# Optimization experiments

Hardware: AMD Instinct MI355X
Metric: run time of the kernel (lower is better)

The kernel has to match this reference:

```python
import jax, jax.numpy as jnp
import numpy as np

N, C, W = 64, 64, 4096
F, WW = 64, 9

def next_power2(n):
    return int(2 ** np.ceil(np.log2(n)))

def setup_inputs() -> dict:
    key = jax.random.key(0)
    k1, k2, k3 = jax.random.split(key, 3)
    x = jax.random.normal(k1, (N, C, W), dtype=jnp.float32)
    filt = jax.random.normal(k2, (F, C, WW), dtype=jnp.float32)
    bias = jax.random.normal(k3, (F,), dtype=jnp.float32)
    return {"x": x, "filt": filt, "bias": bias}

def reference(x, filt, bias):
    # FFT-based valid cross-correlation, no spectral compression
    # (preserve_energy_rate=None, index_back=None, out_size=None, padding=None).
    n_, c_, w_ = x.shape
    f_, _, ww_ = filt.shape
    out_W = w_ - ww_ + 1  # valid correlation output length
    fftsize = next_power2(w_ + ww_ - 1)
    xf = jnp.fft.rfft(x, n=fftsize)            # [N, C, K] complex64
    wf = jnp.fft.rfft(filt, n=fftsize)         # [F, C, K] complex64
    # correlation = ifft(Xf * conj(Wf)); sum over channels in freq domain
    of = jnp.einsum('nck,fck->nfk', xf, jnp.conj(wf))  # [N, F, K]
    out = jnp.fft.irfft(of, n=fftsize)[..., :out_W]    # [N, F, out_W] float32
    # original adds bias[f] once per channel iteration -> C * bias
    out = out + (c_ * bias)[None, :, None]
    return out
```

## Files before the change

### kernel.cpp

```cpp
#include <hip/hip_runtime.h>
#include <stdint.h>

#define N_   64
#define C_   64
#define W_   4096
#define F_   64
#define WW_  9
#define OW_  4088
#define WBLK 64
#define WROWS 72

typedef __bf16 bf16x8 __attribute__((ext_vector_type(8)));
typedef float  f32x4  __attribute__((ext_vector_type(4)));

__device__ __forceinline__ unsigned short f2bf(float f) {
    union { float f; uint32_t u; } v; v.f = f;
    uint32_t u = v.u;
    return (unsigned short)((u + 0x7FFFu + ((u >> 16) & 1u)) >> 16);
}

__device__ __forceinline__ uint2 pk4(float a, float b, float c, float d) {
    uint2 r;
    asm volatile("v_cvt_pk_bf16_f32 %0, %1, %2" : "=v"(r.x) : "v"(a), "v"(b));
    asm volatile("v_cvt_pk_bf16_f32 %0, %1, %2" : "=v"(r.y) : "v"(c), "v"(d));
    return r;
}

__global__ __launch_bounds__(256) void prep_filt_k(const float* __restrict__ filt,
                                                   unsigned short* __restrict__ filtB) {
    int id = blockIdx.x * 256 + threadIdx.x;
    if (id < WW_ * F_ * C_) {
        int j    = id & 7;
        int lane = (id >> 3) & 63;
        int uu   = (id >> 9) & 3;
        int m    = (id >> 11) & 1;
        int t    = id >> 12;
        int l15  = lane & 15, lg = lane >> 4;
        int f = uu * 16 + l15;
        int c = m * 32 + lg * 8 + j;
        filtB[id] = f2bf(filt[(f * C_ + c) * WW_ + t]);
    }
}

__global__ __launch_bounds__(64, 3) void conv_k(const float* __restrict__ x,
                                                const unsigned short* __restrict__ filtB,
                                                const float* __restrict__ bias,
                                                float* __restrict__ out) {
    __shared__ unsigned short xs[WROWS * 64];

    const int lane = threadIdx.x;
    const int n    = blockIdx.y;
    const int w0   = blockIdx.x * WBLK;
    const int l15  = lane & 15;
    const int lg   = lane >> 4;

    {
        const int wq = l15 << 2;
        const int cs = (lg << 2) & 7;
        const float* xb = x + ((size_t)(n * C_ + (lg << 2))) * W_ + w0 + wq;
        #pragma unroll
        for (int i = 0; i < 4; ++i) {
            const float* xi = xb + (size_t)(i * 16) * W_;
            float4 r0 = *reinterpret_cast<const float4*>(xi);
            float4 r1 = *reinterpret_cast<const float4*>(xi + W_);
            float4 r2 = *reinterpret_cast<const float4*>(xi + 2 * W_);
            float4 r3 = *reinterpret_cast<const float4*>(xi + 3 * W_);
            const int cg = (lg >> 1) + (i << 1);
            const float* p0 = &r0.x; const float* p1 = &r1.x;
            const float* p2 = &r2.x; const float* p3 = &r3.x;
            #pragma unroll
            for (int jj = 0; jj < 4; ++jj) {
                int w = wq + jj;
                uint2 u2 = pk4(p0[jj], p1[jj], p2[jj], p3[jj]);
                *reinterpret_cast<uint2*>(&xs[w * 64 + ((cg ^ (w & 7)) << 3) + cs]) = u2;
            }
        }
        if (lane < 32) {
            const int hc4 = (lane >> 1) << 2;
            const int hw  = 64 + ((lane & 1) << 2);
            const int hcg = hc4 >> 3;
            const int hcs = hc4 & 7;
            const float* hp = x + ((size_t)(n * C_ + hc4)) * W_ + w0 + hw;
            #pragma unroll
            for (int jj = 0; jj < 4; ++jj) {
                int w  = hw + jj;
                int gw = w0 + w;
                float a0 = 0.f, a1 = 0.f, a2 = 0.f, a3 = 0.f;
                if (gw < W_) {
                    a0 = hp[jj];
                    a1 = hp[jj + (size_t)W_];
                    a2 = hp[jj + (size_t)2 * W_];
                    a3 = hp[jj + (size_t)3 * W_];
                }
                uint2 u2 = pk4(a0, a1, a2, a3);
                *reinterpret_cast<uint2*>(&xs[w * 64 + ((hcg ^ (w & 7)) << 3) + hcs]) = u2;
            }
        }
    }

    const unsigned short* Bb = filtB + lane * 8;

    float bv[4];
    #pragma unroll
    for (int uu = 0; uu < 4; ++uu)
        bv[uu] = 64.0f * bias[uu * 16 + l15];

    f32x4 acc[4][4];
    #pragma unroll
    for (int s = 0; s < 4; ++s)
        #pragma unroll
        for (int uu = 0; uu < 4; ++uu)
            acc[s][uu] = (f32x4){0.f, 0.f, 0.f, 0.f};

    #pragma unroll
    for (int t = 0; t < WW_; ++t) {
        #pragma unroll
        for (int m = 0; m < 2; ++m) {
            bf16x8 a[4];
            #pragma unroll
            for (int s = 0; s < 4; ++s) {
                int row   = s * 16 + l15 + t;
                int chunk = ((m << 2) | lg) ^ (row & 7);
                a[s] = *reinterpret_cast<const bf16x8*>(&xs[row * 64 + chunk * 8]);
            }
            bf16x8 b[4];
            #pragma unroll
            for (int uu = 0; uu < 4; ++uu)
                b[uu] = *reinterpret_cast<const bf16x8*>(Bb + (((t * 2 + m) * 4 + uu) << 9));
            __builtin_amdgcn_s_setprio(1);
            #pragma unroll
            for (int s = 0; s < 4; ++s)
                #pragma unroll
                for (int uu = 0; uu < 4; ++uu)
                    acc[s][uu] = __builtin_amdgcn_mfma_f32_16x16x32_bf16(a[s], b[uu], acc[s][uu], 0, 0, 0);
            __builtin_amdgcn_s_setprio(0);
        }
    }

    #pragma unroll
    for (int uu = 0; uu < 4; ++uu) {
        const int f = uu * 16 + l15;
        #pragma unroll
        for (int s = 0; s < 4; ++s) {
            int wg = w0 + s * 16 + lg * 4;
            if (wg < OW_) {
                float4 o;
                o.x = acc[s][uu][0] + bv[uu];
                o.y = acc[s][uu][1] + bv[uu];
                o.z = acc[s][uu][2] + bv[uu];
                o.w = acc[s][uu][3] + bv[uu];
                *reinterpret_cast<float4*>(out + ((size_t)(n * F_ + f) * OW_ + wg)) = o;
            }
        }
    }
}

extern "C" void kernel_launch(void* const* d_in, const int* in_sizes, int n_in,
                              void* d_out, int out_size, void* d_ws, size_t ws_size,
                              hipStream_t stream) {
    const float* x    = (const float*)d_in[0];
    const float* filt = (const float*)d_in[1];
    const float* bias = (const float*)d_in[2];
    float* out        = (float*)d_out;

    unsigned short* filtB = (unsigned short*)d_ws;

    prep_filt_k<<<(WW_ * F_ * C_ + 255) / 256, 256, 0, stream>>>(filt, filtB);

    dim3 grid(W_ / WBLK, N_);
    conv_k<<<grid, 64, 0, stream>>>(x, filtB, bias, out);
}
```

Measured before the change: 48.79 us.

## Use two-wave blocks over 128-wide tiles and prefetch filter fragments

Each block now covers 128 output positions with two wavefronts sharing one LDS tile of x, which cuts the redundant halo loads per output and halves the block count. A __syncthreads is added because the waves cooperatively fill LDS. Filter fragments for the next (t,m) step are loaded one step ahead into a second set of registers, so global load latency overlaps the MFMAs. This adds register pressure from the extra buffer and a block-level barrier, and it changes occupancy.

```diff
diff --git a/kernel.cpp b/kernel.cpp
--- a/kernel.cpp
+++ b/kernel.cpp
@@ -7,8 +7,8 @@
 #define F_   64
 #define WW_  9
 #define OW_  4088
-#define WBLK 64
-#define WROWS 72
+#define WBLK 128
+#define WROWS 136
 
 typedef __bf16 bf16x8 __attribute__((ext_vector_type(8)));
 typedef float  f32x4  __attribute__((ext_vector_type(4)));
@@ -42,30 +42,33 @@
     }
 }
 
-__global__ __launch_bounds__(64, 3) void conv_k(const float* __restrict__ x,
-                                                const unsigned short* __restrict__ filtB,
-                                                const float* __restrict__ bias,
-                                                float* __restrict__ out) {
+__global__ __launch_bounds__(128, 3) void conv_k(const float* __restrict__ x,
+                                                 const unsigned short* __restrict__ filtB,
+                                                 const float* __restrict__ bias,
+                                                 float* __restrict__ out) {
     __shared__ unsigned short xs[WROWS * 64];
 
-    const int lane = threadIdx.x;
+    const int tid  = threadIdx.x;
+    const int lane = tid & 63;
+    const int wv   = tid >> 6;
     const int n    = blockIdx.y;
     const int w0   = blockIdx.x * WBLK;
     const int l15  = lane & 15;
     const int lg   = lane >> 4;
 
     {
-        const int wq = l15 << 2;
-        const int cs = (lg << 2) & 7;
-        const float* xb = x + ((size_t)(n * C_ + (lg << 2))) * W_ + w0 + wq;
+        const int wq    = (tid & 31) << 2;
+        const int cbase = (tid >> 5) << 2;
         #pragma unroll
         for (int i = 0; i < 4; ++i) {
-            const float* xi = xb + (size_t)(i * 16) * W_;
-            float4 r0 = *reinterpret_cast<const float4*>(xi);
-            float4 r1 = *reinterpret_cast<const float4*>(xi + W_);
-            float4 r2 = *reinterpret_cast<const float4*>(xi + 2 * W_);
-            float4 r3 = *reinterpret_cast<const float4*>(xi + 3 * W_);
-            const int cg = (lg >> 1) + (i << 1);
+            const int c4 = cbase + (i << 4);
+            const float* xb = x + ((size_t)(n * C_ + c4)) * W_ + w0 + wq;
+            float4 r0 = *reinterpret_cast<const float4*>(xb);
+            float4 r1 = *reinterpret_cast<const float4*>(xb + W_);
+            float4 r2 = *reinterpret_cast<const float4*>(xb + 2 * W_);
+            float4 r3 = *reinterpret_cast<const float4*>(xb + 3 * W_);
+            const int cg = c4 >> 3;
+            const int cs = c4 & 7;
             const float* p0 = &r0.x; const float* p1 = &r1.x;
             const float* p2 = &r2.x; const float* p3 = &r3.x;
             #pragma unroll
@@ -75,29 +78,31 @@
                 *reinterpret_cast<uint2*>(&xs[w * 64 + ((cg ^ (w & 7)) << 3) + cs]) = u2;
             }
         }
-        if (lane < 32) {
-            const int hc4 = (lane >> 1) << 2;
-            const int hw  = 64 + ((lane & 1) << 2);
+        if (tid < 32) {
+            const int hc4 = (tid & 15) << 2;
+            const int hwl = 128 + ((tid >> 4) << 2);
             const int hcg = hc4 >> 3;
             const int hcs = hc4 & 7;
-            const float* hp = x + ((size_t)(n * C_ + hc4)) * W_ + w0 + hw;
             #pragma unroll
             for (int jj = 0; jj < 4; ++jj) {
-                int w  = hw + jj;
+                int w  = hwl + jj;
                 int gw = w0 + w;
                 float a0 = 0.f, a1 = 0.f, a2 = 0.f, a3 = 0.f;
                 if (gw < W_) {
-                    a0 = hp[jj];
-                    a1 = hp[jj + (size_t)W_];
-                    a2 = hp[jj + (size_t)2 * W_];
-                    a3 = hp[jj + (size_t)3 * W_];
+                    const float* hp = x + ((size_t)(n * C_ + hc4)) * W_ + gw;
+                    a0 = hp[0];
+                    a1 = hp[(size_t)W_];
+                    a2 = hp[(size_t)2 * W_];
+                    a3 = hp[(size_t)3 * W_];
                 }
                 uint2 u2 = pk4(a0, a1, a2, a3);
                 *reinterpret_cast<uint2*>(&xs[w * 64 + ((hcg ^ (w & 7)) << 3) + hcs]) = u2;
             }
         }
     }
+    __syncthreads();
 
+    const int wvb = wv << 6;
     const unsigned short* Bb = filtB + lane * 8;
 
     float bv[4];
@@ -112,28 +117,37 @@
         for (int uu = 0; uu < 4; ++uu)
             acc[s][uu] = (f32x4){0.f, 0.f, 0.f, 0.f};
 
+    bf16x8 Bc[4], Bn[4];
+    #pragma unroll
+    for (int u = 0; u < 4; ++u)
+        Bc[u] = *reinterpret_cast<const bf16x8*>(Bb + (u << 9));
+
     #pragma unroll
     for (int t = 0; t < WW_; ++t) {
         #pragma unroll
         for (int m = 0; m < 2; ++m) {
+            const int step = t * 2 + m;
+            if (step < 17) {
+                #pragma unroll
+                for (int u = 0; u < 4; ++u)
+                    Bn[u] = *reinterpret_cast<const bf16x8*>(Bb + (((step + 1) * 4 + u) << 9));
+            }
             bf16x8 a[4];
             #pragma unroll
             for (int s = 0; s < 4; ++s) {
-                int row   = s * 16 + l15 + t;
+                int row   = wvb + s * 16 + l15 + t;
                 int chunk = ((m << 2) | lg) ^ (row & 7);
                 a[s] = *reinterpret_cast<const bf16x8*>(&xs[row * 64 + chunk * 8]);
             }
-            bf16x8 b[4];
-            #pragma unroll
-            for (int uu = 0; uu < 4; ++uu)
-                b[uu] = *reinterpret_cast<const bf16x8*>(Bb + (((t * 2 + m) * 4 + uu) << 9));
             __builtin_amdgcn_s_setprio(1);
             #pragma unroll
             for (int s = 0; s < 4; ++s)
                 #pragma unroll
-                for (int uu = 0; uu < 4; ++uu)
-                    acc[s][uu] = __builtin_amdgcn_mfma_f32_16x16x32_bf16(a[s], b[uu], acc[s][uu], 0, 0, 0);
+                for (int u = 0; u < 4; ++u)
+                    acc[s][u] = __builtin_amdgcn_mfma_f32_16x16x32_bf16(a[s], Bc[u], acc[s][u], 0, 0, 0);
             __builtin_amdgcn_s_setprio(0);
+            #pragma unroll
+            for (int u = 0; u < 4; ++u) Bc[u] = Bn[u];
         }
     }
 
@@ -142,7 +156,7 @@
         const int f = uu * 16 + l15;
         #pragma unroll
         for (int s = 0; s < 4; ++s) {
-            int wg = w0 + s * 16 + lg * 4;
+            int wg = w0 + wvb + s * 16 + lg * 4;
             if (wg < OW_) {
                 float4 o;
                 o.x = acc[s][uu][0] + bv[uu];
@@ -168,5 +182,5 @@
     prep_filt_k<<<(WW_ * F_ * C_ + 255) / 256, 256, 0, stream>>>(filt, filtB);
 
     dim3 grid(W_ / WBLK, N_);
-    conv_k<<<grid, 64, 0, stream>>>(x, filtB, bias, out);
+    conv_k<<<grid, 128, 0, stream>>>(x, filtB, bias, out);
 }
```

Measured after the change: 45.30 us. 1.08x faster.
